# Kernel optimization log

Hardware: AMD Instinct MI355X
Metric: run time of the kernel (lower is better)

The kernel has to match this reference:

```python
import jax, jax.numpy as jnp
import numpy as np

L, H, P = 32768, 256, 256
DT_MIN, DT_MAX = 0.001, 0.1


def setup_inputs() -> dict:
    key = jax.random.key(0)
    ks = jax.random.split(key, 7)
    signal = jax.random.normal(ks[0], (L, H), jnp.float32)
    # stable HiPPO-like init: negative real part, random imaginary part
    lam_re = -(0.1 + 0.4 * jax.random.uniform(ks[1], (P,), jnp.float32))
    lam_im = jax.random.normal(ks[2], (P,), jnp.float32)
    Lambda_ri = jnp.stack([lam_re, lam_im], axis=-1)            # (P, 2)
    B_ri = jax.random.normal(ks[3], (P, H, 2), jnp.float32) / np.float32(np.sqrt(H))
    C_ri = jax.random.normal(ks[4], (H, P, 2), jnp.float32) / np.float32(np.sqrt(P))
    D = jax.random.uniform(ks[5], (H,), jnp.float32)
    log_step = jnp.log(DT_MIN + (DT_MAX - DT_MIN) * jax.random.uniform(ks[6], (P,), jnp.float32))
    return {"signal": signal, "Lambda_ri": Lambda_ri, "B_ri": B_ri,
            "C_ri": C_ri, "D": D, "log_step": log_step}


def reference(signal, Lambda_ri, B_ri, C_ri, D, log_step):
    # --- get_BC_tilde (bcInit='dense'): B stored real (P,H,2) -> complex ---
    Lambda = jax.lax.complex(Lambda_ri[..., 0], Lambda_ri[..., 1])   # (P,)
    B_tilde = jax.lax.complex(B_ri[..., 0], B_ri[..., 1])            # (P, H)
    C_tilde = jax.lax.complex(C_ri[..., 0], C_ri[..., 1])            # (H, P)

    # --- discretize_zoh ---
    step = jnp.exp(log_step)                                          # (P,) step_scale = 1.0
    Lambda_bar = jnp.exp(Lambda * step)                               # (P,) complex
    B_bar = ((Lambda_bar - 1.0) / Lambda)[:, None] * B_tilde          # (P, H) complex

    # --- apply_ssm: Bu_elements = vmap(u -> B_bar @ u) over time ---
    Bu = signal.astype(Lambda_bar.dtype) @ B_bar.T                    # (L, P) complex
    Lam = jnp.broadcast_to(Lambda_bar, Bu.shape)                      # (L, P)

    def binop(qi, qj):
        A_i, Bu_i = qi
        A_j, Bu_j = qj
        return (A_j * A_i, Bu_j + A_j * Bu_i)

    _, xs = jax.lax.associative_scan(binop, (Lam, Bu), axis=0)        # (L, P)

    # y = Re(C_tilde @ x) + D * u, vectorized over time
    y = jnp.real(xs @ C_tilde.T) + D * signal                         # (L, H)
    return y
```

## Files before the change

### kernel.cpp

```cpp
#include <hip/hip_runtime.h>
#include <math.h>

constexpr int L = 32768;
constexpr int H = 256;
constexpr int P = 256;
constexpr int T = 64;
constexpr int NC = L / T;
constexpr int N1 = 2 * P;
constexpr int LDA = 40;
constexpr int LDEP = 130;

typedef __attribute__((ext_vector_type(8))) short short8;
typedef __attribute__((ext_vector_type(4))) float f32x4;

__device__ __forceinline__ unsigned f2bf(float f) {
  unsigned u = __float_as_uint(f);
  return (u + 0x7FFFu + ((u >> 16) & 1u)) >> 16;
}
__device__ __forceinline__ float bf_lo(unsigned u) { return __uint_as_float(u << 16); }
__device__ __forceinline__ float bf_hi(unsigned u) { return __uint_as_float(u & 0xFFFF0000u); }

__device__ __forceinline__ void gload_lds16(const unsigned short* g, unsigned short* l) {
  __builtin_amdgcn_global_load_lds(
      (const __attribute__((address_space(1))) unsigned int*)(g),
      (__attribute__((address_space(3))) unsigned int*)(l), 16, 0, 0);
}

#define KBAR(N) do { \
    asm volatile("s_waitcnt vmcnt(" #N ") lgkmcnt(0)" ::: "memory"); \
    __builtin_amdgcn_s_barrier(); \
    __builtin_amdgcn_sched_barrier(0); \
  } while (0)

#define VMEM_FENCE() __builtin_amdgcn_sched_barrier(0x38F)

__device__ __forceinline__ void lambda_bar_of(const float* __restrict__ lam,
                                              const float* __restrict__ lstep,
                                              int p, float& lbr, float& lbi) {
  float lr = lam[2 * p], li = lam[2 * p + 1];
  float st = expf(lstep[p]);
  float ea = expf(lr * st);
  lbr = ea * cosf(li * st);
  lbi = ea * sinf(li * st);
}

__global__ __launch_bounds__(256) void k_prep(const float* __restrict__ lam,
                                              const float* __restrict__ lstep,
                                              const float* __restrict__ Bri,
                                              const float* __restrict__ Cri,
                                              unsigned short* __restrict__ Bcat,
                                              unsigned short* __restrict__ Ccat,
                                              float* __restrict__ powr,
                                              float* __restrict__ powi) {
  int idx = blockIdx.x * 256 + threadIdx.x;
  if (idx < N1 * H) {
    int n = idx >> 8, k = idx & 255;
    int p = n >> 1, comp = n & 1;
    float lr = lam[2 * p], li = lam[2 * p + 1];
    float st = expf(lstep[p]);
    float ea = expf(lr * st);
    float lbr = ea * cosf(li * st), lbi = ea * sinf(li * st);
    float inv = 1.0f / (lr * lr + li * li);
    float nr = lbr - 1.0f;
    float fr = (nr * lr + lbi * li) * inv;
    float fi = (lbi * lr - nr * li) * inv;
    float br = Bri[2 * (p * H + k)], bi = Bri[2 * (p * H + k) + 1];
    float v = (comp == 0) ? (fr * br - fi * bi) : (fr * bi + fi * br);
    Bcat[idx] = (unsigned short)f2bf(v);
  } else if (idx < 2 * N1 * H) {
    int j = idx - N1 * H;
    int h = j >> 9, k2 = j & 511;
    int p = k2 >> 1;
    float v = ((k2 & 1) == 0) ? Cri[2 * (h * P + p)] : -Cri[2 * (h * P + p) + 1];
    Ccat[j] = (unsigned short)f2bf(v);
  } else {
    int r = idx - 2 * N1 * H;
    int t = r >> 8, p = r & 255;
    float lr = lam[2 * p], li = lam[2 * p + 1];
    float st = expf(lstep[p]);
    float e = (float)(t + 1);
    float er = expf(e * lr * st);
    powr[r] = er * cosf(e * li * st);
    powi[r] = er * sinf(e * li * st);
  }
}

__global__ __launch_bounds__(256, 4) void k_gemm1s(const float* __restrict__ sig,
                                                   const unsigned short* __restrict__ Bcat,
                                                   const float* __restrict__ lam,
                                                   const float* __restrict__ lstep,
                                                   unsigned short* __restrict__ Xl,
                                                   float* __restrict__ Sr,
                                                   float* __restrict__ Si) {
  constexpr int K = 256, NIT = K / 32;
  __shared__ __align__(16) char smem[36864];
  unsigned short* sA[2] = {(unsigned short*)smem, (unsigned short*)smem + 5120};
  unsigned short* sB[2] = {(unsigned short*)smem + 10240, (unsigned short*)smem + 14336};
  float* sEpi = (float*)smem;
  const int tid = threadIdx.x;
  const int lane = tid & 63;
  const int wave = tid >> 6;
  const int wr = (wave >> 1) * 64, wc = (wave & 1) * 64;
  const int m0 = blockIdx.x * 128, n0 = blockIdx.y * 128;
  const int ar = tid >> 1, aq = (tid & 1) * 16;
  const int brow = ((tid >> 6) << 4) | (tid & 15);
  const int bko = ((tid >> 4) & 3) * 8;
  const int frow = lane & 15, fk = (lane >> 4) * 8;
  const int hb = (wave & 1) * 2048;
  f32x4 acc[4][4];
#pragma unroll
  for (int i = 0; i < 4; i++)
#pragma unroll
    for (int j = 0; j < 4; j++) acc[i][j] = (f32x4){0.f, 0.f, 0.f, 0.f};

  float4 aR0[4], aR1[4];
  const float* abase = sig + (size_t)(m0 + ar) * K + aq;
#define LOAD_A(R, k0) { const float* s_ = abase + (k0); \
    R[0] = *(const float4*)(s_); R[1] = *(const float4*)(s_ + 4); \
    R[2] = *(const float4*)(s_ + 8); R[3] = *(const float4*)(s_ + 12); }
#define WRITE_A(R, dst) { uint4 w0, w1; \
    w0.x = f2bf(R[0].x) | (f2bf(R[0].y) << 16); w0.y = f2bf(R[0].z) | (f2bf(R[0].w) << 16); \
    w0.z = f2bf(R[1].x) | (f2bf(R[1].y) << 16); w0.w = f2bf(R[1].z) | (f2bf(R[1].w) << 16); \
    w1.x = f2bf(R[2].x) | (f2bf(R[2].y) << 16); w1.y = f2bf(R[2].z) | (f2bf(R[2].w) << 16); \
    w1.z = f2bf(R[3].x) | (f2bf(R[3].y) << 16); w1.w = f2bf(R[3].z) | (f2bf(R[3].w) << 16); \
    *(uint4*)((dst) + ar * LDA + aq) = w0; *(uint4*)((dst) + ar * LDA + aq + 8) = w1; }
#define ISSUE_B(k0, buf) { \
    gload_lds16(Bcat + (size_t)(n0 + brow) * K + (k0) + bko, sB[buf] + tid * 8); \
    gload_lds16(Bcat + (size_t)(n0 + 64 + brow) * K + (k0) + bko, sB[buf] + 2048 + tid * 8); }

  LOAD_A(aR0, 0);
  LOAD_A(aR1, 32);
  VMEM_FENCE();
  ISSUE_B(0, 0);
  VMEM_FENCE();
  WRITE_A(aR0, sA[0]);
  LOAD_A(aR0, 64);
  KBAR(4);
#pragma unroll
  for (int it = 0; it < NIT; it++) {
    const int cur = it & 1, nxt = cur ^ 1;
    if (it + 1 < NIT) {
      if (((it + 1) & 1) == 0) { WRITE_A(aR0, sA[nxt]); } else { WRITE_A(aR1, sA[nxt]); }
      ISSUE_B((it + 1) * 32, nxt);
    }
    VMEM_FENCE();
    if (it + 3 < NIT) {
      if (((it + 3) & 1) == 0) { LOAD_A(aR0, (it + 3) * 32); } else { LOAD_A(aR1, (it + 3) * 32); }
    }
    short8 af[4], bfr[4];
#pragma unroll
    for (int i = 0; i < 4; i++) af[i] = *(const short8*)(sA[cur] + (wr + i * 16 + frow) * LDA + fk);
#pragma unroll
    for (int j = 0; j < 4; j++) bfr[j] = *(const short8*)(sB[cur] + hb + (j * 64 + lane) * 8);
#pragma unroll
    for (int i = 0; i < 4; i++)
#pragma unroll
      for (int j = 0; j < 4; j++)
        acc[i][j] = __builtin_amdgcn_mfma_f32_16x16x32_bf16(af[i], bfr[j], acc[i][j], 0, 0, 0);
    if (it + 1 < NIT) {
      if (it + 3 < NIT) { KBAR(4); } else { KBAR(0); }
    }
  }
  __syncthreads();

  const int crow = (lane >> 4) * 4, ccol = wc + (lane & 15);
#pragma unroll
  for (int half = 0; half < 2; half++) {
    if ((wave >> 1) == half) {
#pragma unroll
      for (int i = 0; i < 4; i++)
#pragma unroll
        for (int j = 0; j < 4; j++)
#pragma unroll
          for (int g = 0; g < 4; g++)
            sEpi[(crow + i * 16 + g) * LDEP + ccol + j * 16] = acc[i][j][g];
    }
    __syncthreads();
    if (tid < 64) {
      const int pl = tid;
      const int gp = (n0 >> 1) + pl;
      const int c = blockIdx.x * 2 + half;
      float lbr, lbi;
      lambda_bar_of(lam, lstep, gp, lbr, lbi);
      float xr = 0.f, xi = 0.f;
      const float* e = sEpi + 2 * pl;
      const size_t gbase = (size_t)(m0 + half * 64) * N1 + n0 + 2 * pl;
      for (int tb = 0; tb < T; tb += 8) {
        float2 v[8];
#pragma unroll
        for (int u = 0; u < 8; u++) v[u] = *(const float2*)(e + (tb + u) * LDEP);
        unsigned ov[8];
#pragma unroll
        for (int u = 0; u < 8; u++) {
          float nr = fmaf(lbr, xr, fmaf(-lbi, xi, v[u].x));
          float ni = fmaf(lbr, xi, fmaf(lbi, xr, v[u].y));
          xr = nr; xi = ni;
          ov[u] = f2bf(xr) | (f2bf(xi) << 16);
        }
#pragma unroll
        for (int u = 0; u < 8; u++)
          *(unsigned*)(Xl + gbase + (size_t)(tb + u) * N1) = ov[u];
      }
      Sr[c * P + gp] = xr;
      Si[c * P + gp] = xi;
    }
    __syncthreads();
  }
#undef LOAD_A
#undef WRITE_A
#undef ISSUE_B
}

__global__ __launch_bounds__(64) void k_carry2(const float* __restrict__ lam,
                                               const float* __restrict__ lstep,
                                               const float* __restrict__ Sr,
                                               const float* __restrict__ Si,
                                               float* __restrict__ car, float* __restrict__ cai) {
  const int p = blockIdx.x;
  const int t = threadIdx.x;
  float lr = lam[2 * p], li = lam[2 * p + 1];
  float st = expf(lstep[p]);
  float eT = expf((float)T * lr * st);
  float lTr = eT * cosf((float)T * li * st);
  float lTi = eT * sinf((float)T * li * st);
  float vr[8], vi[8];
#pragma unroll
  for (int u = 0; u < 8; u++) {
    vr[u] = Sr[(t * 8 + u) * P + p];
    vi[u] = Si[(t * 8 + u) * P + p];
  }
  float Br = 0.f, Bi = 0.f;
#pragma unroll
  for (int u = 0; u < 8; u++) {
    float nr = fmaf(lTr, Br, fmaf(-lTi, Bi, vr[u]));
    float ni = fmaf(lTr, Bi, fmaf(lTi, Br, vi[u]));
    Br = nr; Bi = ni;
  }
  float e8 = expf(8.0f * (float)T * lr * st);
  float Ar = e8 * cosf(8.0f * (float)T * li * st);
  float Ai = e8 * sinf(8.0f * (float)T * li * st);
#pragma unroll
  for (int d = 1; d < 64; d <<= 1) {
    float Aor = __shfl_up(Ar, d), Aoi = __shfl_up(Ai, d);
    float Bor = __shfl_up(Br, d), Boi = __shfl_up(Bi, d);
    if (t >= d) {
      float nBr = Ar * Bor - Ai * Boi + Br;
      float nBi = Ar * Boi + Ai * Bor + Bi;
      float nAr = Aor * Ar - Aoi * Ai;
      float nAi = Aor * Ai + Aoi * Ar;
      Br = nBr; Bi = nBi; Ar = nAr; Ai = nAi;
    }
  }
  float cr = __shfl_up(Br, 1), ci = __shfl_up(Bi, 1);
  if (t == 0) { cr = 0.f; ci = 0.f; }
#pragma unroll
  for (int u = 0; u < 8; u++) {
    car[(t * 8 + u) * P + p] = cr;
    cai[(t * 8 + u) * P + p] = ci;
    float nr = fmaf(lTr, cr, fmaf(-lTi, ci, vr[u]));
    float ni = fmaf(lTr, ci, fmaf(lTi, cr, vi[u]));
    cr = nr; ci = ni;
  }
}

__global__ __launch_bounds__(256) void k_gemm2f(const unsigned short* __restrict__ Xl,
                                                const unsigned short* __restrict__ Ccat,
                                                const float* __restrict__ powr,
                                                const float* __restrict__ powi,
                                                const float* __restrict__ car,
                                                const float* __restrict__ cai,
                                                const float* __restrict__ sig,
                                                const float* __restrict__ Dv,
                                                float* __restrict__ out) {
  constexpr int K = 512, NIT = K / 32;
  __shared__ __align__(16) char smem[36864];
  unsigned short* sA[2] = {(unsigned short*)smem, (unsigned short*)smem + 5120};
  unsigned short* sB[2] = {(unsigned short*)smem + 10240, (unsigned short*)smem + 14336};
  const int tid = threadIdx.x;
  const int lane = tid & 63;
  const int wave = tid >> 6;
  const int wr = (wave >> 1) * 64, wc = (wave & 1) * 64;
  const int m0 = blockIdx.x * 128, n0 = blockIdx.y * 128;
  const int ar = tid >> 1, aq = (tid & 1) * 16;
  const int t_ = ar & 63;
  const int cc = blockIdx.x * 2 + (ar >> 6);
  const int brow = ((tid >> 6) << 4) | (tid & 15);
  const int bko = ((tid >> 4) & 3) * 8;
  const int frow = lane & 15, fk = (lane >> 4) * 8;
  const int hb = (wave & 1) * 2048;
  f32x4 acc[4][4];
#pragma unroll
  for (int i = 0; i < 4; i++)
#pragma unroll
    for (int j = 0; j < 4; j++) acc[i][j] = (f32x4){0.f, 0.f, 0.f, 0.f};

  uint4 x0a, x1a, x0b, x1b;
  float4 pr0, pr1, pi0, pi1, cr0, cr1, ci0, ci1;
  const unsigned short* xbase = Xl + (size_t)(m0 + ar) * N1 + aq;
  const float* prb = powr + t_ * P;
  const float* pib = powi + t_ * P;
  const float* crb = car + cc * P;
  const float* cib = cai + cc * P;
#define LOAD_X(A0, A1, k0) { \
    A0 = *(const uint4*)(xbase + (k0)); A1 = *(const uint4*)(xbase + (k0) + 8); }
#define LOAD_PC(k0) { const int p0_ = ((k0) >> 1) + (tid & 1) * 8; \
    pr0 = *(const float4*)(prb + p0_); pr1 = *(const float4*)(prb + p0_ + 4); \
    pi0 = *(const float4*)(pib + p0_); pi1 = *(const float4*)(pib + p0_ + 4); \
    cr0 = *(const float4*)(crb + p0_); cr1 = *(const float4*)(crb + p0_ + 4); \
    ci0 = *(const float4*)(cib + p0_); ci1 = *(const float4*)(cib + p0_ + 4); }
#define WRITE_A2(XA, XB, dst) { \
    unsigned xw[8] = {XA.x, XA.y, XA.z, XA.w, XB.x, XB.y, XB.z, XB.w}; \
    float pr_[8] = {pr0.x, pr0.y, pr0.z, pr0.w, pr1.x, pr1.y, pr1.z, pr1.w}; \
    float pi_[8] = {pi0.x, pi0.y, pi0.z, pi0.w, pi1.x, pi1.y, pi1.z, pi1.w}; \
    float cr_[8] = {cr0.x, cr0.y, cr0.z, cr0.w, cr1.x, cr1.y, cr1.z, cr1.w}; \
    float ci_[8] = {ci0.x, ci0.y, ci0.z, ci0.w, ci1.x, ci1.y, ci1.z, ci1.w}; \
    unsigned wo[8]; \
    _Pragma("unroll") for (int j_ = 0; j_ < 8; j_++) { \
      float xgr = bf_lo(xw[j_]) + (pr_[j_] * cr_[j_] - pi_[j_] * ci_[j_]); \
      float xgi = bf_hi(xw[j_]) + (pr_[j_] * ci_[j_] + pi_[j_] * cr_[j_]); \
      wo[j_] = f2bf(xgr) | (f2bf(xgi) << 16); } \
    uint4 w0, w1; \
    w0.x = wo[0]; w0.y = wo[1]; w0.z = wo[2]; w0.w = wo[3]; \
    w1.x = wo[4]; w1.y = wo[5]; w1.z = wo[6]; w1.w = wo[7]; \
    *(uint4*)((dst) + ar * LDA + aq) = w0; *(uint4*)((dst) + ar * LDA + aq + 8) = w1; }
#define ISSUE_B2(k0, buf) { \
    gload_lds16(Ccat + (size_t)(n0 + brow) * K + (k0) + bko, sB[buf] + tid * 8); \
    gload_lds16(Ccat + (size_t)(n0 + 64 + brow) * K + (k0) + bko, sB[buf] + 2048 + tid * 8); }

  LOAD_X(x0a, x1a, 0);
  LOAD_X(x0b, x1b, 32);
  LOAD_PC(0);
  VMEM_FENCE();
  ISSUE_B2(0, 0);
  VMEM_FENCE();
  WRITE_A2(x0a, x1a, sA[0]);
  LOAD_X(x0a, x1a, 64);
  LOAD_PC(32);
  KBAR(10);
#pragma unroll
  for (int it = 0; it < NIT; it++) {
    const int cur = it & 1, nxt = cur ^ 1;
    if (it + 1 < NIT) {
      if (((it + 1) & 1) == 0) { WRITE_A2(x0a, x1a, sA[nxt]); } else { WRITE_A2(x0b, x1b, sA[nxt]); }
      ISSUE_B2((it + 1) * 32, nxt);
    }
    VMEM_FENCE();
    if (it + 3 < NIT) {
      if (((it + 3) & 1) == 0) { LOAD_X(x0a, x1a, (it + 3) * 32); } else { LOAD_X(x0b, x1b, (it + 3) * 32); }
    }
    if (it + 2 < NIT) LOAD_PC((it + 2) * 32);
    short8 af[4], bfr[4];
#pragma unroll
    for (int i = 0; i < 4; i++) af[i] = *(const short8*)(sA[cur] + (wr + i * 16 + frow) * LDA + fk);
#pragma unroll
    for (int j = 0; j < 4; j++) bfr[j] = *(const short8*)(sB[cur] + hb + (j * 64 + lane) * 8);
#pragma unroll
    for (int i = 0; i < 4; i++)
#pragma unroll
      for (int j = 0; j < 4; j++)
        acc[i][j] = __builtin_amdgcn_mfma_f32_16x16x32_bf16(af[i], bfr[j], acc[i][j], 0, 0, 0);
    if (it + 1 < NIT) {
      if (it + 3 < NIT) { KBAR(10); }
      else if (it + 2 < NIT) { KBAR(8); }
      else { KBAR(0); }
    }
  }

  const int crow = wr + (lane >> 4) * 4, ccol = wc + (lane & 15);
  float dcol[4];
#pragma unroll
  for (int j = 0; j < 4; j++) dcol[j] = Dv[n0 + ccol + j * 16];
#pragma unroll
  for (int i = 0; i < 4; i++)
#pragma unroll
    for (int j = 0; j < 4; j++) {
      int col = n0 + ccol + j * 16;
#pragma unroll
      for (int g = 0; g < 4; g++) {
        int row = m0 + crow + i * 16 + g;
        out[(size_t)row * H + col] = acc[i][j][g] + dcol[j] * sig[(size_t)row * H + col];
      }
    }
#undef LOAD_X
#undef LOAD_PC
#undef WRITE_A2
#undef ISSUE_B2
}

extern "C" void kernel_launch(void* const* d_in, const int* in_sizes, int n_in,
                              void* d_out, int out_size, void* d_ws, size_t ws_size,
                              hipStream_t stream) {
  const float* sig = (const float*)d_in[0];
  const float* lam = (const float*)d_in[1];
  const float* Bri = (const float*)d_in[2];
  const float* Cri = (const float*)d_in[3];
  const float* Dv  = (const float*)d_in[4];
  const float* lst = (const float*)d_in[5];
  float* out = (float*)d_out;

  unsigned short* Bcat = (unsigned short*)d_ws;
  unsigned short* Ccat = Bcat + (size_t)N1 * H;
  unsigned short* Xl   = Ccat + (size_t)H * N1;
  float* powr = (float*)(Xl + (size_t)L * N1);
  float* powi = powr + T * P;
  float* Sr   = powi + T * P;
  float* Si   = Sr + NC * P;
  float* car  = Si + NC * P;
  float* cai  = car + NC * P;

  k_prep<<<(2 * N1 * H + T * P) / 256, 256, 0, stream>>>(lam, lst, Bri, Cri,
                                                         Bcat, Ccat, powr, powi);
  dim3 g1(L / 128, N1 / 128);
  k_gemm1s<<<g1, 256, 0, stream>>>(sig, Bcat, lam, lst, Xl, Sr, Si);
  k_carry2<<<NC / 2, 64, 0, stream>>>(lam, lst, Sr, Si, car, cai);
  dim3 g2(L / 128, H / 128);
  k_gemm2f<<<g2, 256, 0, stream>>>(Xl, Ccat, powr, powi, car, cai, sig, Dv, out);
}
```

Measured before the change: 150.8 us.

## Deepen B-operand pipeline to four LDS stages and transpose chunk-state layout

Both GEMM kernels now prefetch the B/C weight tiles three iterations ahead into a four-slot LDS ring instead of double-buffering. The gemm2 kernel also double-buffers the power/carry loads alongside X, and the vmcnt waits are retuned to match. The chunk-end states Sr/Si are stored transposed (p-major), so the carry kernel reads them with contiguous float4 loads instead of strided scalar loads. This raises LDS per block and lowers the occupancy hint to 3, trading occupancy for deeper latency hiding.

```diff
diff --git a/kernel.cpp b/kernel.cpp
--- a/kernel.cpp
+++ b/kernel.cpp
@@ -85,7 +85,7 @@
   }
 }
 
-__global__ __launch_bounds__(256, 4) void k_gemm1s(const float* __restrict__ sig,
+__global__ __launch_bounds__(256, 3) void k_gemm1s(const float* __restrict__ sig,
                                                    const unsigned short* __restrict__ Bcat,
                                                    const float* __restrict__ lam,
                                                    const float* __restrict__ lstep,
@@ -93,9 +93,10 @@
                                                    float* __restrict__ Sr,
                                                    float* __restrict__ Si) {
   constexpr int K = 256, NIT = K / 32;
-  __shared__ __align__(16) char smem[36864];
+  __shared__ __align__(16) char smem[53248];
   unsigned short* sA[2] = {(unsigned short*)smem, (unsigned short*)smem + 5120};
-  unsigned short* sB[2] = {(unsigned short*)smem + 10240, (unsigned short*)smem + 14336};
+  unsigned short* sB[4] = {(unsigned short*)(smem + 20480), (unsigned short*)(smem + 28672),
+                           (unsigned short*)(smem + 36864), (unsigned short*)(smem + 45056)};
   float* sEpi = (float*)smem;
   const int tid = threadIdx.x;
   const int lane = tid & 63;
@@ -132,33 +133,39 @@
   LOAD_A(aR1, 32);
   VMEM_FENCE();
   ISSUE_B(0, 0);
+  ISSUE_B(32, 1);
+  ISSUE_B(64, 2);
   VMEM_FENCE();
   WRITE_A(aR0, sA[0]);
   LOAD_A(aR0, 64);
-  KBAR(4);
+  VMEM_FENCE();
+  KBAR(8);
 #pragma unroll
   for (int it = 0; it < NIT; it++) {
-    const int cur = it & 1, nxt = cur ^ 1;
     if (it + 1 < NIT) {
-      if (((it + 1) & 1) == 0) { WRITE_A(aR0, sA[nxt]); } else { WRITE_A(aR1, sA[nxt]); }
-      ISSUE_B((it + 1) * 32, nxt);
+      if (((it + 1) & 1) == 0) { WRITE_A(aR0, sA[0]); } else { WRITE_A(aR1, sA[1]); }
     }
     VMEM_FENCE();
     if (it + 3 < NIT) {
       if (((it + 3) & 1) == 0) { LOAD_A(aR0, (it + 3) * 32); } else { LOAD_A(aR1, (it + 3) * 32); }
     }
+    VMEM_FENCE();
+    if (it + 3 < NIT) ISSUE_B((it + 3) * 32, (it + 3) & 3);
+    VMEM_FENCE();
     short8 af[4], bfr[4];
 #pragma unroll
-    for (int i = 0; i < 4; i++) af[i] = *(const short8*)(sA[cur] + (wr + i * 16 + frow) * LDA + fk);
-#pragma unroll
-    for (int j = 0; j < 4; j++) bfr[j] = *(const short8*)(sB[cur] + hb + (j * 64 + lane) * 8);
+    for (int i = 0; i < 4; i++) af[i] = *(const short8*)(sA[it & 1] + (wr + i * 16 + frow) * LDA + fk);
+#pragma unroll
+    for (int j = 0; j < 4; j++) bfr[j] = *(const short8*)(sB[it & 3] + hb + (j * 64 + lane) * 8);
 #pragma unroll
     for (int i = 0; i < 4; i++)
 #pragma unroll
       for (int j = 0; j < 4; j++)
         acc[i][j] = __builtin_amdgcn_mfma_f32_16x16x32_bf16(af[i], bfr[j], acc[i][j], 0, 0, 0);
     if (it + 1 < NIT) {
-      if (it + 3 < NIT) { KBAR(4); } else { KBAR(0); }
+      if (it < NIT - 3) { KBAR(12); }
+      else if (it == NIT - 3) { KBAR(6); }
+      else { KBAR(0); }
     }
   }
   __syncthreads();
@@ -201,8 +208,8 @@
         for (int u = 0; u < 8; u++)
           *(unsigned*)(Xl + gbase + (size_t)(tb + u) * N1) = ov[u];
       }
-      Sr[c * P + gp] = xr;
-      Si[c * P + gp] = xi;
+      Sr[(size_t)gp * NC + c] = xr;
+      Si[(size_t)gp * NC + c] = xi;
     }
     __syncthreads();
   }
@@ -224,10 +231,15 @@
   float lTr = eT * cosf((float)T * li * st);
   float lTi = eT * sinf((float)T * li * st);
   float vr[8], vi[8];
-#pragma unroll
-  for (int u = 0; u < 8; u++) {
-    vr[u] = Sr[(t * 8 + u) * P + p];
-    vi[u] = Si[(t * 8 + u) * P + p];
+  {
+    const float* srp = Sr + (size_t)p * NC + t * 8;
+    const float* sip = Si + (size_t)p * NC + t * 8;
+    float4 a0 = *(const float4*)(srp), a1 = *(const float4*)(srp + 4);
+    float4 b0 = *(const float4*)(sip), b1 = *(const float4*)(sip + 4);
+    vr[0] = a0.x; vr[1] = a0.y; vr[2] = a0.z; vr[3] = a0.w;
+    vr[4] = a1.x; vr[5] = a1.y; vr[6] = a1.z; vr[7] = a1.w;
+    vi[0] = b0.x; vi[1] = b0.y; vi[2] = b0.z; vi[3] = b0.w;
+    vi[4] = b1.x; vi[5] = b1.y; vi[6] = b1.z; vi[7] = b1.w;
   }
   float Br = 0.f, Bi = 0.f;
 #pragma unroll
@@ -263,19 +275,20 @@
   }
 }
 
-__global__ __launch_bounds__(256) void k_gemm2f(const unsigned short* __restrict__ Xl,
-                                                const unsigned short* __restrict__ Ccat,
-                                                const float* __restrict__ powr,
-                                                const float* __restrict__ powi,
-                                                const float* __restrict__ car,
-                                                const float* __restrict__ cai,
-                                                const float* __restrict__ sig,
-                                                const float* __restrict__ Dv,
-                                                float* __restrict__ out) {
+__global__ __launch_bounds__(256, 3) void k_gemm2f(const unsigned short* __restrict__ Xl,
+                                                   const unsigned short* __restrict__ Ccat,
+                                                   const float* __restrict__ powr,
+                                                   const float* __restrict__ powi,
+                                                   const float* __restrict__ car,
+                                                   const float* __restrict__ cai,
+                                                   const float* __restrict__ sig,
+                                                   const float* __restrict__ Dv,
+                                                   float* __restrict__ out) {
   constexpr int K = 512, NIT = K / 32;
-  __shared__ __align__(16) char smem[36864];
+  __shared__ __align__(16) char smem[53248];
   unsigned short* sA[2] = {(unsigned short*)smem, (unsigned short*)smem + 5120};
-  unsigned short* sB[2] = {(unsigned short*)smem + 10240, (unsigned short*)smem + 14336};
+  unsigned short* sB[4] = {(unsigned short*)(smem + 20480), (unsigned short*)(smem + 28672),
+                           (unsigned short*)(smem + 36864), (unsigned short*)(smem + 45056)};
   const int tid = threadIdx.x;
   const int lane = tid & 63;
   const int wave = tid >> 6;
@@ -295,7 +308,8 @@
     for (int j = 0; j < 4; j++) acc[i][j] = (f32x4){0.f, 0.f, 0.f, 0.f};
 
   uint4 x0a, x1a, x0b, x1b;
-  float4 pr0, pr1, pi0, pi1, cr0, cr1, ci0, ci1;
+  float4 pra0, pra1, pia0, pia1, cra0, cra1, cia0, cia1;
+  float4 prb0, prb1, pib0, pib1, crb0, crb1, cib0, cib1;
   const unsigned short* xbase = Xl + (size_t)(m0 + ar) * N1 + aq;
   const float* prb = powr + t_ * P;
   const float* pib = powi + t_ * P;
@@ -303,17 +317,18 @@
   const float* cib = cai + cc * P;
 #define LOAD_X(A0, A1, k0) { \
     A0 = *(const uint4*)(xbase + (k0)); A1 = *(const uint4*)(xbase + (k0) + 8); }
-#define LOAD_PC(k0) { const int p0_ = ((k0) >> 1) + (tid & 1) * 8; \
-    pr0 = *(const float4*)(prb + p0_); pr1 = *(const float4*)(prb + p0_ + 4); \
-    pi0 = *(const float4*)(pib + p0_); pi1 = *(const float4*)(pib + p0_ + 4); \
-    cr0 = *(const float4*)(crb + p0_); cr1 = *(const float4*)(crb + p0_ + 4); \
-    ci0 = *(const float4*)(cib + p0_); ci1 = *(const float4*)(cib + p0_ + 4); }
-#define WRITE_A2(XA, XB, dst) { \
+#define LOAD_PC(PR0, PR1, PI0, PI1, CR0, CR1, CI0, CI1, k0) { \
+    const int p0_ = ((k0) >> 1) + (tid & 1) * 8; \
+    PR0 = *(const float4*)(prb + p0_); PR1 = *(const float4*)(prb + p0_ + 4); \
+    PI0 = *(const float4*)(pib + p0_); PI1 = *(const float4*)(pib + p0_ + 4); \
+    CR0 = *(const float4*)(crb + p0_); CR1 = *(const float4*)(crb + p0_ + 4); \
+    CI0 = *(const float4*)(cib + p0_); CI1 = *(const float4*)(cib + p0_ + 4); }
+#define WRITE_A2(XA, XB, PR0, PR1, PI0, PI1, CR0, CR1, CI0, CI1, dst) { \
     unsigned xw[8] = {XA.x, XA.y, XA.z, XA.w, XB.x, XB.y, XB.z, XB.w}; \
-    float pr_[8] = {pr0.x, pr0.y, pr0.z, pr0.w, pr1.x, pr1.y, pr1.z, pr1.w}; \
-    float pi_[8] = {pi0.x, pi0.y, pi0.z, pi0.w, pi1.x, pi1.y, pi1.z, pi1.w}; \
-    float cr_[8] = {cr0.x, cr0.y, cr0.z, cr0.w, cr1.x, cr1.y, cr1.z, cr1.w}; \
-    float ci_[8] = {ci0.x, ci0.y, ci0.z, ci0.w, ci1.x, ci1.y, ci1.z, ci1.w}; \
+    float pr_[8] = {PR0.x, PR0.y, PR0.z, PR0.w, PR1.x, PR1.y, PR1.z, PR1.w}; \
+    float pi_[8] = {PI0.x, PI0.y, PI0.z, PI0.w, PI1.x, PI1.y, PI1.z, PI1.w}; \
+    float cr_[8] = {CR0.x, CR0.y, CR0.z, CR0.w, CR1.x, CR1.y, CR1.z, CR1.w}; \
+    float ci_[8] = {CI0.x, CI0.y, CI0.z, CI0.w, CI1.x, CI1.y, CI1.z, CI1.w}; \
     unsigned wo[8]; \
     _Pragma("unroll") for (int j_ = 0; j_ < 8; j_++) { \
       float xgr = bf_lo(xw[j_]) + (pr_[j_] * cr_[j_] - pi_[j_] * ci_[j_]); \
@@ -328,40 +343,54 @@
     gload_lds16(Ccat + (size_t)(n0 + 64 + brow) * K + (k0) + bko, sB[buf] + 2048 + tid * 8); }
 
   LOAD_X(x0a, x1a, 0);
+  LOAD_PC(pra0, pra1, pia0, pia1, cra0, cra1, cia0, cia1, 0);
   LOAD_X(x0b, x1b, 32);
-  LOAD_PC(0);
+  LOAD_PC(prb0, prb1, pib0, pib1, crb0, crb1, cib0, cib1, 32);
   VMEM_FENCE();
   ISSUE_B2(0, 0);
-  VMEM_FENCE();
-  WRITE_A2(x0a, x1a, sA[0]);
+  ISSUE_B2(32, 1);
+  ISSUE_B2(64, 2);
+  VMEM_FENCE();
+  WRITE_A2(x0a, x1a, pra0, pra1, pia0, pia1, cra0, cra1, cia0, cia1, sA[0]);
   LOAD_X(x0a, x1a, 64);
-  LOAD_PC(32);
-  KBAR(10);
+  LOAD_PC(pra0, pra1, pia0, pia1, cra0, cra1, cia0, cia1, 64);
+  VMEM_FENCE();
+  KBAR(14);
 #pragma unroll
   for (int it = 0; it < NIT; it++) {
-    const int cur = it & 1, nxt = cur ^ 1;
     if (it + 1 < NIT) {
-      if (((it + 1) & 1) == 0) { WRITE_A2(x0a, x1a, sA[nxt]); } else { WRITE_A2(x0b, x1b, sA[nxt]); }
-      ISSUE_B2((it + 1) * 32, nxt);
+      if (((it + 1) & 1) == 0) {
+        WRITE_A2(x0a, x1a, pra0, pra1, pia0, pia1, cra0, cra1, cia0, cia1, sA[0]);
+      } else {
+        WRITE_A2(x0b, x1b, prb0, prb1, pib0, pib1, crb0, crb1, cib0, cib1, sA[1]);
+      }
     }
     VMEM_FENCE();
     if (it + 3 < NIT) {
-      if (((it + 3) & 1) == 0) { LOAD_X(x0a, x1a, (it + 3) * 32); } else { LOAD_X(x0b, x1b, (it + 3) * 32); }
-    }
-    if (it + 2 < NIT) LOAD_PC((it + 2) * 32);
+      if (((it + 3) & 1) == 0) {
+        LOAD_X(x0a, x1a, (it + 3) * 32);
+        LOAD_PC(pra0, pra1, pia0, pia1, cra0, cra1, cia0, cia1, (it + 3) * 32);
+      } else {
+        LOAD_X(x0b, x1b, (it + 3) * 32);
+        LOAD_PC(prb0, prb1, pib0, pib1, crb0, crb1, cib0, cib1, (it + 3) * 32);
+      }
+    }
+    VMEM_FENCE();
+    if (it + 3 < NIT) ISSUE_B2((it + 3) * 32, (it + 3) & 3);
+    VMEM_FENCE();
     short8 af[4], bfr[4];
 #pragma unroll
-    for (int i = 0; i < 4; i++) af[i] = *(const short8*)(sA[cur] + (wr + i * 16 + frow) * LDA + fk);
-#pragma unroll
-    for (int j = 0; j < 4; j++) bfr[j] = *(const short8*)(sB[cur] + hb + (j * 64 + lane) * 8);
+    for (int i = 0; i < 4; i++) af[i] = *(const short8*)(sA[it & 1] + (wr + i * 16 + frow) * LDA + fk);
+#pragma unroll
+    for (int j = 0; j < 4; j++) bfr[j] = *(const short8*)(sB[it & 3] + hb + (j * 64 + lane) * 8);
 #pragma unroll
     for (int i = 0; i < 4; i++)
 #pragma unroll
       for (int j = 0; j < 4; j++)
         acc[i][j] = __builtin_amdgcn_mfma_f32_16x16x32_bf16(af[i], bfr[j], acc[i][j], 0, 0, 0);
     if (it + 1 < NIT) {
-      if (it + 3 < NIT) { KBAR(10); }
-      else if (it + 2 < NIT) { KBAR(8); }
+      if (it < NIT - 3) { KBAR(24); }
+      else if (it == NIT - 3) { KBAR(12); }
       else { KBAR(0); }
     }
   }
```

Result: slower. 161.1 us (+6.8%).
